# Performance work log

Measured on AMD Instinct MI355X. Metric: run time of the kernel, lower is better.

The kernel has to match this reference:

```python
import jax, jax.numpy as jnp
import numpy as np

N_NODES = 100000
N_EDGES = 3200000
D_IN = 256
D_OUT = 256


def setup_inputs() -> dict:
    key = jax.random.key(0)
    k1, k2, k3, k4, k5 = jax.random.split(key, 5)
    x = jax.random.normal(k1, (N_NODES, D_IN), dtype=jnp.float32)
    # xavier-uniform-like init for weight
    limit = float(np.sqrt(6.0 / (D_IN + D_OUT)))
    weight = jax.random.uniform(k2, (D_IN, D_OUT), dtype=jnp.float32, minval=-limit, maxval=limit)
    edge_val = jax.random.uniform(k3, (N_EDGES,), dtype=jnp.float32)
    edge_row = jax.random.randint(k4, (N_EDGES,), 0, N_NODES, dtype=jnp.int32)
    edge_col = jax.random.randint(k5, (N_EDGES,), 0, N_NODES, dtype=jnp.int32)
    return {"x": x, "weight": weight, "edge_val": edge_val,
            "edge_row": edge_row, "edge_col": edge_col}


def reference(x, weight, edge_val, edge_row, edge_col):
    # dropout p=0.0 -> identity
    support = x @ weight                                  # [N, D_OUT]
    # spmm: out[r] += val * support[c] for each edge (r, c, val)
    msgs = support[edge_col] * edge_val[:, None]          # [E, D_OUT]
    out = jax.ops.segment_sum(msgs, edge_row, num_segments=N_NODES)
    return jax.nn.relu(out)
```

## Files before the change

### kernel.cpp

```cpp
#include <hip/hip_runtime.h>

#define N_NODES 100000
#define N_EDGES 3200000
#define D 256
#define OVF_MAX 8192

#define RPB 128
#define NBUCK 782
#define CAPB 5120
#define SCAP 4608

#define CHUNK 4096
#define NBLK_A ((N_EDGES + CHUNK - 1) / CHUNK)
#define NGRP 196

#define CAST_BLOCKS 6250
#define GEMM_BLOCKS (N_NODES / 16)

typedef __attribute__((ext_vector_type(8))) short bf16x8;
typedef __attribute__((ext_vector_type(4))) float f32x4;

__device__ unsigned short g_wtp[(size_t)16 * 8 * 64 * 8];
__device__ unsigned short g_xb[(size_t)N_NODES * D];
__device__ unsigned       g_y[(size_t)N_NODES * (D / 2)];
__device__ int   g_bucket_cur[NBUCK];
__device__ int2  g_binned[(size_t)NBUCK * CAPB];
__device__ int   g_novf;
__device__ int   g_ovf_row[OVF_MAX];
__device__ int2  g_ovf_edge[OVF_MAX];

__device__ __forceinline__ unsigned short f2bf(float f) {
    unsigned u = __float_as_uint(f);
    unsigned r = u + 0x7fffu + ((u >> 16) & 1u);
    return (unsigned short)(r >> 16);
}

__global__ void setup_kernel(const float* __restrict__ W) {
    const int tid = threadIdx.x;
    if (blockIdx.x < 64) {
        int pb = (blockIdx.x * 256 + tid) * 4;
        #pragma unroll
        for (int j = 0; j < 4; ++j) {
            int p    = pb + j;
            int i8   = p & 7;
            int lane = (p >> 3) & 63;
            int s    = (p >> 9) & 7;
            int nt   = p >> 12;
            int n = nt * 16 + (lane & 15);
            int k = s * 32 + (lane >> 4) * 8 + i8;
            g_wtp[p] = f2bf(W[(size_t)k * D + n]);
        }
    }
    for (int i = blockIdx.x * blockDim.x + tid; i < NBUCK;
         i += gridDim.x * blockDim.x)
        g_bucket_cur[i] = 0;
    if (blockIdx.x == 0 && tid == 0) g_novf = 0;
}

__launch_bounds__(256)
__global__ void bin_cast_kernel(const float* __restrict__ x,
                                const float* __restrict__ edge_val,
                                const int* __restrict__ edge_row,
                                const int* __restrict__ edge_col) {
    __shared__ int2 rec[CHUNK];
    __shared__ unsigned short bid[CHUNK];
    __shared__ int cnt[NGRP * 4];
    __shared__ int pre[NBUCK + 1];
    __shared__ int bas[NBUCK];
    __shared__ int gs[NGRP];
    __shared__ int gofs[NGRP];
    const int tid = threadIdx.x;
    const int b = blockIdx.x;

    if (b < NBLK_A) {
        const int e0 = b * CHUNK;
        for (int q = tid; q < NGRP * 4; q += 256) cnt[q] = 0;
        __syncthreads();
        #pragma unroll
        for (int j = 0; j < CHUNK / 256; ++j) {
            int e = e0 + tid + j * 256;
            if (e < N_EDGES) atomicAdd(&cnt[edge_row[e] >> 7], 1);
        }
        __syncthreads();
        if (tid < NGRP) {
            const int* c = &cnt[tid * 4];
            gs[tid] = c[0] + c[1] + c[2] + c[3];
        }
        __syncthreads();
        if (tid < NGRP) {
            int s = 0;
            for (int j = 0; j < tid; ++j) s += gs[j];
            gofs[tid] = s;
        }
        __syncthreads();
        for (int q = tid; q < NBUCK; q += 256) {
            int p = gofs[q >> 2];
            for (int j = q & ~3; j < q; ++j) p += cnt[j];
            pre[q] = p;
        }
        if (tid == 0) pre[NBUCK] = gofs[NGRP - 1] + gs[NGRP - 1];
        __syncthreads();
        for (int q = tid; q < NBUCK; q += 256)
            bas[q] = cnt[q] ? atomicAdd(&g_bucket_cur[q], cnt[q]) : 0;
        __syncthreads();
        for (int q = tid; q < NGRP * 4; q += 256) cnt[q] = 0;
        __syncthreads();
        #pragma unroll
        for (int j = 0; j < CHUNK / 256; ++j) {
            int e = e0 + tid + j * 256;
            if (e < N_EDGES) {
                int r = edge_row[e];
                int q = r >> 7;
                int o = atomicAdd(&cnt[q], 1);
                int pos = pre[q] + o;
                int2 pk;
                pk.x = edge_col[e] | ((r & 127) << 17);
                pk.y = __float_as_int(edge_val[e]);
                rec[pos] = pk;
                bid[pos] = (unsigned short)q;
            }
        }
        __syncthreads();
        const int total = pre[NBUCK];
        for (int i = tid; i < total; i += 256) {
            int q = bid[i];
            int dest = bas[q] + (i - pre[q]);
            int2 pk = rec[i];
            if (dest < CAPB) {
                g_binned[(size_t)q * CAPB + dest] = pk;
            } else {
                int o = atomicAdd(&g_novf, 1);
                if (o < OVF_MAX) {
                    g_ovf_row[o] = (q << 7) | (pk.x >> 17);
                    int2 ov; ov.x = pk.x & 0x1FFFF; ov.y = pk.y;
                    g_ovf_edge[o] = ov;
                }
            }
        }
    } else {
        const size_t base = (size_t)(b - NBLK_A) * 4096 + (size_t)tid * 16;
        const float4* xp = (const float4*)&x[base];
        float4 f0 = xp[0], f1 = xp[1], f2 = xp[2], f3 = xp[3];
        unsigned short o[16];
        o[ 0]=f2bf(f0.x); o[ 1]=f2bf(f0.y); o[ 2]=f2bf(f0.z); o[ 3]=f2bf(f0.w);
        o[ 4]=f2bf(f1.x); o[ 5]=f2bf(f1.y); o[ 6]=f2bf(f1.z); o[ 7]=f2bf(f1.w);
        o[ 8]=f2bf(f2.x); o[ 9]=f2bf(f2.y); o[10]=f2bf(f2.z); o[11]=f2bf(f2.w);
        o[12]=f2bf(f3.x); o[13]=f2bf(f3.y); o[14]=f2bf(f3.z); o[15]=f2bf(f3.w);
        uint4* dst = (uint4*)&g_xb[base];
        dst[0] = *(const uint4*)&o[0];
        dst[1] = *(const uint4*)&o[8];
    }
}

__launch_bounds__(512)
__global__ void spmm_kernel() {
    __shared__ int2 srec[SCAP];
    __shared__ int rcnt[RPB];
    __shared__ int rofs[RPB];
    __shared__ int rcur[RPB];
    const int k   = blockIdx.x;
    const int tid = threadIdx.x;
    const int nrec_all = min(g_bucket_cur[k], CAPB);
    const int nstage   = min(nrec_all, SCAP);
    const int2* src = &g_binned[(size_t)k * CAPB];

    if (tid < RPB) { rcnt[tid] = 0; rcur[tid] = 0; }
    __syncthreads();
    for (int i = tid; i < nstage; i += 512)
        atomicAdd(&rcnt[src[i].x >> 17], 1);
    __syncthreads();
    if (tid < RPB) {
        int s = 0;
        for (int j = 0; j < tid; ++j) s += rcnt[j];
        rofs[tid] = s;
    }
    __syncthreads();
    for (int i = tid; i < nstage; i += 512) {
        int2 pk = src[i];
        int rl  = pk.x >> 17;
        int pos = rofs[rl] + atomicAdd(&rcur[rl], 1);
        srec[pos] = pk;
    }
    __syncthreads();

    const int grp = tid >> 7;
    const int t   = tid & 127;
    const unsigned* xb = (const unsigned*)g_xb;
    const int novf = min(g_novf, OVF_MAX);

    for (int rr = 0; rr < 32; ++rr) {
        const int rl  = grp * 32 + rr;
        const int row = k * RPB + rl;
        if (row >= N_NODES) break;
        const int cnt = rcnt[rl];
        const int ofs = rofs[rl];
        float a0 = 0.f, a1 = 0.f;
        int i = 0;
        for (; i + 3 < cnt; i += 4) {
            int2 e0 = srec[ofs + i];
            int2 e1 = srec[ofs + i + 1];
            int2 e2 = srec[ofs + i + 2];
            int2 e3 = srec[ofs + i + 3];
            unsigned p0 = xb[(size_t)(e0.x & 0x1FFFF) * (D / 2) + t];
            unsigned p1 = xb[(size_t)(e1.x & 0x1FFFF) * (D / 2) + t];
            unsigned p2 = xb[(size_t)(e2.x & 0x1FFFF) * (D / 2) + t];
            unsigned p3 = xb[(size_t)(e3.x & 0x1FFFF) * (D / 2) + t];
            float v0 = __int_as_float(e0.y);
            float v1 = __int_as_float(e1.y);
            float v2 = __int_as_float(e2.y);
            float v3 = __int_as_float(e3.y);
            a0 += v0 * __uint_as_float(p0 << 16);
            a1 += v0 * __uint_as_float(p0 & 0xffff0000u);
            a0 += v1 * __uint_as_float(p1 << 16);
            a1 += v1 * __uint_as_float(p1 & 0xffff0000u);
            a0 += v2 * __uint_as_float(p2 << 16);
            a1 += v2 * __uint_as_float(p2 & 0xffff0000u);
            a0 += v3 * __uint_as_float(p3 << 16);
            a1 += v3 * __uint_as_float(p3 & 0xffff0000u);
        }
        for (; i < cnt; ++i) {
            int2 e0 = srec[ofs + i];
            unsigned p0 = xb[(size_t)(e0.x & 0x1FFFF) * (D / 2) + t];
            float v0 = __int_as_float(e0.y);
            a0 += v0 * __uint_as_float(p0 << 16);
            a1 += v0 * __uint_as_float(p0 & 0xffff0000u);
        }
        for (int j = nstage; j < nrec_all; ++j) {
            int2 pk = src[j];
            if ((pk.x >> 17) == rl) {
                unsigned p0 = xb[(size_t)(pk.x & 0x1FFFF) * (D / 2) + t];
                float v0 = __int_as_float(pk.y);
                a0 += v0 * __uint_as_float(p0 << 16);
                a1 += v0 * __uint_as_float(p0 & 0xffff0000u);
            }
        }
        if (novf > 0) {
            for (int j = 0; j < novf; ++j) {
                if (g_ovf_row[j] == row) {
                    int2 ee = g_ovf_edge[j];
                    float v0 = __int_as_float(ee.y);
                    unsigned p0 = xb[(size_t)ee.x * (D / 2) + t];
                    a0 += v0 * __uint_as_float(p0 << 16);
                    a1 += v0 * __uint_as_float(p0 & 0xffff0000u);
                }
            }
        }
        g_y[(size_t)row * (D / 2) + t] =
            (unsigned)f2bf(a0) | ((unsigned)f2bf(a1) << 16);
    }
}

__launch_bounds__(256)
__global__ void gemm_kernel(float* __restrict__ out) {
    __shared__ float tile[4][16][68];
    const int g    = blockIdx.x;
    const int wave = threadIdx.x >> 6;
    const int lane = threadIdx.x & 63;
    const int m0   = g * 16;
    const int n0   = wave * 64;
    const int lm   = lane & 15;
    const int q    = lane >> 4;

    const unsigned short* Yb = (const unsigned short*)g_y;
    f32x4 acc0 = {}, acc1 = {}, acc2 = {}, acc3 = {};

    #pragma unroll
    for (int s = 0; s < 8; ++s) {
        bf16x8 av = *(const bf16x8*)&Yb[(size_t)(m0 + lm) * D + s * 32 + q * 8];
        const unsigned short* bp =
            &g_wtp[((size_t)(wave * 4) * 8 + s) * 512 + lane * 8];
        bf16x8 b0 = *(const bf16x8*)&bp[0 * 4096];
        bf16x8 b1 = *(const bf16x8*)&bp[1 * 4096];
        bf16x8 b2 = *(const bf16x8*)&bp[2 * 4096];
        bf16x8 b3 = *(const bf16x8*)&bp[3 * 4096];
        acc0 = __builtin_amdgcn_mfma_f32_16x16x32_bf16(av, b0, acc0, 0, 0, 0);
        acc1 = __builtin_amdgcn_mfma_f32_16x16x32_bf16(av, b1, acc1, 0, 0, 0);
        acc2 = __builtin_amdgcn_mfma_f32_16x16x32_bf16(av, b2, acc2, 0, 0, 0);
        acc3 = __builtin_amdgcn_mfma_f32_16x16x32_bf16(av, b3, acc3, 0, 0, 0);
    }

    #pragma unroll
    for (int r = 0; r < 4; ++r) {
        tile[wave][q * 4 + r][ 0 + lm] = acc0[r];
        tile[wave][q * 4 + r][16 + lm] = acc1[r];
        tile[wave][q * 4 + r][32 + lm] = acc2[r];
        tile[wave][q * 4 + r][48 + lm] = acc3[r];
    }
    const int row  = lane >> 2;
    const int cseg = (lane & 3) * 16;
    float ov[16];
    #pragma unroll
    for (int j = 0; j < 16; ++j)
        ov[j] = fmaxf(tile[wave][row][cseg + j], 0.f);
    float* dst = &out[(size_t)(m0 + row) * D + n0 + cseg];
    #pragma unroll
    for (int j = 0; j < 4; ++j)
        __builtin_nontemporal_store(*(const f32x4*)&ov[j * 4], (f32x4*)&dst[j * 4]);
}

extern "C" void kernel_launch(void* const* d_in, const int* in_sizes, int n_in,
                              void* d_out, int out_size, void* d_ws, size_t ws_size,
                              hipStream_t stream) {
    const float* x        = (const float*)d_in[0];
    const float* weight   = (const float*)d_in[1];
    const float* edge_val = (const float*)d_in[2];
    const int*   edge_row = (const int*)d_in[3];
    const int*   edge_col = (const int*)d_in[4];
    float* out = (float*)d_out;

    setup_kernel<<<64, 256, 0, stream>>>(weight);
    bin_cast_kernel<<<NBLK_A + CAST_BLOCKS, 256, 0, stream>>>(x, edge_val, edge_row, edge_col);
    spmm_kernel<<<NBUCK, 512, 0, stream>>>();
    gemm_kernel<<<GEMM_BLOCKS, 256, 0, stream>>>(out);
}
```

Before: 655.8 us.

## Replace bucketed binning with per-row padded ELL slots via global atomics

Replaces the two-pass, shared-memory bucket sort of edges (782 buckets, with a per-block counting sort inside spmm) with a direct per-row padded layout. Each edge claims a slot with a global atomicAdd on its destination row's cursor, and anything past 64 slots goes to an overflow list. spmm now runs one 128-thread block per row, reading that row's slots directly with nontemporal loads. This removes the shared-memory staging and scan overhead, at the cost of 3.2M contended global atomics, scattered 8-byte writes into a large padded array, and 100k small blocks.

```diff
diff --git a/kernel.cpp b/kernel.cpp
--- a/kernel.cpp
+++ b/kernel.cpp
@@ -3,17 +3,10 @@
 #define N_NODES 100000
 #define N_EDGES 3200000
 #define D 256
+#define CAP 64
 #define OVF_MAX 8192
 
-#define RPB 128
-#define NBUCK 782
-#define CAPB 5120
-#define SCAP 4608
-
-#define CHUNK 4096
-#define NBLK_A ((N_EDGES + CHUNK - 1) / CHUNK)
-#define NGRP 196
-
+#define BUILD_BLOCKS 3125
 #define CAST_BLOCKS 6250
 #define GEMM_BLOCKS (N_NODES / 16)
 
@@ -23,8 +16,8 @@
 __device__ unsigned short g_wtp[(size_t)16 * 8 * 64 * 8];
 __device__ unsigned short g_xb[(size_t)N_NODES * D];
 __device__ unsigned       g_y[(size_t)N_NODES * (D / 2)];
-__device__ int   g_bucket_cur[NBUCK];
-__device__ int2  g_binned[(size_t)NBUCK * CAPB];
+__device__ int   g_cursor[N_NODES];
+__device__ int2  g_pad[(size_t)N_NODES * CAP];
 __device__ int   g_novf;
 __device__ int   g_ovf_row[OVF_MAX];
 __device__ int2  g_ovf_edge[OVF_MAX];
@@ -51,94 +44,39 @@
             g_wtp[p] = f2bf(W[(size_t)k * D + n]);
         }
     }
-    for (int i = blockIdx.x * blockDim.x + tid; i < NBUCK;
+    for (int i = blockIdx.x * blockDim.x + tid; i < N_NODES;
          i += gridDim.x * blockDim.x)
-        g_bucket_cur[i] = 0;
+        g_cursor[i] = 0;
     if (blockIdx.x == 0 && tid == 0) g_novf = 0;
 }
 
 __launch_bounds__(256)
-__global__ void bin_cast_kernel(const float* __restrict__ x,
-                                const float* __restrict__ edge_val,
-                                const int* __restrict__ edge_row,
-                                const int* __restrict__ edge_col) {
-    __shared__ int2 rec[CHUNK];
-    __shared__ unsigned short bid[CHUNK];
-    __shared__ int cnt[NGRP * 4];
-    __shared__ int pre[NBUCK + 1];
-    __shared__ int bas[NBUCK];
-    __shared__ int gs[NGRP];
-    __shared__ int gofs[NGRP];
+__global__ void build_cast_kernel(const float* __restrict__ x,
+                                  const float* __restrict__ edge_val,
+                                  const int* __restrict__ edge_row,
+                                  const int* __restrict__ edge_col) {
     const int tid = threadIdx.x;
     const int b = blockIdx.x;
 
-    if (b < NBLK_A) {
-        const int e0 = b * CHUNK;
-        for (int q = tid; q < NGRP * 4; q += 256) cnt[q] = 0;
-        __syncthreads();
+    if (b < BUILD_BLOCKS) {
+        const int e0 = b * 1024;
         #pragma unroll
-        for (int j = 0; j < CHUNK / 256; ++j) {
-            int e = e0 + tid + j * 256;
-            if (e < N_EDGES) atomicAdd(&cnt[edge_row[e] >> 7], 1);
-        }
-        __syncthreads();
-        if (tid < NGRP) {
-            const int* c = &cnt[tid * 4];
-            gs[tid] = c[0] + c[1] + c[2] + c[3];
-        }
-        __syncthreads();
-        if (tid < NGRP) {
-            int s = 0;
-            for (int j = 0; j < tid; ++j) s += gs[j];
-            gofs[tid] = s;
-        }
-        __syncthreads();
-        for (int q = tid; q < NBUCK; q += 256) {
-            int p = gofs[q >> 2];
-            for (int j = q & ~3; j < q; ++j) p += cnt[j];
-            pre[q] = p;
-        }
-        if (tid == 0) pre[NBUCK] = gofs[NGRP - 1] + gs[NGRP - 1];
-        __syncthreads();
-        for (int q = tid; q < NBUCK; q += 256)
-            bas[q] = cnt[q] ? atomicAdd(&g_bucket_cur[q], cnt[q]) : 0;
-        __syncthreads();
-        for (int q = tid; q < NGRP * 4; q += 256) cnt[q] = 0;
-        __syncthreads();
-        #pragma unroll
-        for (int j = 0; j < CHUNK / 256; ++j) {
-            int e = e0 + tid + j * 256;
-            if (e < N_EDGES) {
-                int r = edge_row[e];
-                int q = r >> 7;
-                int o = atomicAdd(&cnt[q], 1);
-                int pos = pre[q] + o;
-                int2 pk;
-                pk.x = edge_col[e] | ((r & 127) << 17);
-                pk.y = __float_as_int(edge_val[e]);
-                rec[pos] = pk;
-                bid[pos] = (unsigned short)q;
-            }
-        }
-        __syncthreads();
-        const int total = pre[NBUCK];
-        for (int i = tid; i < total; i += 256) {
-            int q = bid[i];
-            int dest = bas[q] + (i - pre[q]);
-            int2 pk = rec[i];
-            if (dest < CAPB) {
-                g_binned[(size_t)q * CAPB + dest] = pk;
+        for (int j = 0; j < 4; ++j) {
+            int e = e0 + j * 256 + tid;
+            int r = edge_row[e];
+            int c = edge_col[e];
+            float v = edge_val[e];
+            int slot = atomicAdd(&g_cursor[r], 1);
+            int2 pk; pk.x = c; pk.y = __float_as_int(v);
+            if (slot < CAP) {
+                g_pad[(size_t)r * CAP + slot] = pk;
             } else {
                 int o = atomicAdd(&g_novf, 1);
-                if (o < OVF_MAX) {
-                    g_ovf_row[o] = (q << 7) | (pk.x >> 17);
-                    int2 ov; ov.x = pk.x & 0x1FFFF; ov.y = pk.y;
-                    g_ovf_edge[o] = ov;
-                }
+                if (o < OVF_MAX) { g_ovf_row[o] = r; g_ovf_edge[o] = pk; }
             }
         }
     } else {
-        const size_t base = (size_t)(b - NBLK_A) * 4096 + (size_t)tid * 16;
+        const size_t base = (size_t)(b - BUILD_BLOCKS) * 4096 + (size_t)tid * 16;
         const float4* xp = (const float4*)&x[base];
         float4 f0 = xp[0], f1 = xp[1], f2 = xp[2], f3 = xp[3];
         unsigned short o[16];
@@ -152,102 +90,60 @@
     }
 }
 
-__launch_bounds__(512)
+__launch_bounds__(128)
 __global__ void spmm_kernel() {
-    __shared__ int2 srec[SCAP];
-    __shared__ int rcnt[RPB];
-    __shared__ int rofs[RPB];
-    __shared__ int rcur[RPB];
-    const int k   = blockIdx.x;
-    const int tid = threadIdx.x;
-    const int nrec_all = min(g_bucket_cur[k], CAPB);
-    const int nstage   = min(nrec_all, SCAP);
-    const int2* src = &g_binned[(size_t)k * CAPB];
-
-    if (tid < RPB) { rcnt[tid] = 0; rcur[tid] = 0; }
-    __syncthreads();
-    for (int i = tid; i < nstage; i += 512)
-        atomicAdd(&rcnt[src[i].x >> 17], 1);
-    __syncthreads();
-    if (tid < RPB) {
-        int s = 0;
-        for (int j = 0; j < tid; ++j) s += rcnt[j];
-        rofs[tid] = s;
-    }
-    __syncthreads();
-    for (int i = tid; i < nstage; i += 512) {
-        int2 pk = src[i];
-        int rl  = pk.x >> 17;
-        int pos = rofs[rl] + atomicAdd(&rcur[rl], 1);
-        srec[pos] = pk;
-    }
-    __syncthreads();
-
-    const int grp = tid >> 7;
-    const int t   = tid & 127;
+    const int r = blockIdx.x;
+    const int t = threadIdx.x;
+    const int deg = g_cursor[r];
+    const int dpad = min(deg, CAP);
+    const long long* rowp = (const long long*)&g_pad[(size_t)r * CAP];
     const unsigned* xb = (const unsigned*)g_xb;
+
+    float a0 = 0.f, a1 = 0.f;
+    int i = 0;
+    for (; i + 3 < dpad; i += 4) {
+        long long q0 = __builtin_nontemporal_load(&rowp[i]);
+        long long q1 = __builtin_nontemporal_load(&rowp[i + 1]);
+        long long q2 = __builtin_nontemporal_load(&rowp[i + 2]);
+        long long q3 = __builtin_nontemporal_load(&rowp[i + 3]);
+        unsigned p0 = xb[(size_t)(int)q0 * (D / 2) + t];
+        unsigned p1 = xb[(size_t)(int)q1 * (D / 2) + t];
+        unsigned p2 = xb[(size_t)(int)q2 * (D / 2) + t];
+        unsigned p3 = xb[(size_t)(int)q3 * (D / 2) + t];
+        float v0 = __int_as_float((int)(q0 >> 32));
+        float v1 = __int_as_float((int)(q1 >> 32));
+        float v2 = __int_as_float((int)(q2 >> 32));
+        float v3 = __int_as_float((int)(q3 >> 32));
+        a0 += v0 * __uint_as_float(p0 << 16);
+        a1 += v0 * __uint_as_float(p0 & 0xffff0000u);
+        a0 += v1 * __uint_as_float(p1 << 16);
+        a1 += v1 * __uint_as_float(p1 & 0xffff0000u);
+        a0 += v2 * __uint_as_float(p2 << 16);
+        a1 += v2 * __uint_as_float(p2 & 0xffff0000u);
+        a0 += v3 * __uint_as_float(p3 << 16);
+        a1 += v3 * __uint_as_float(p3 & 0xffff0000u);
+    }
+    for (; i < dpad; ++i) {
+        long long q0 = __builtin_nontemporal_load(&rowp[i]);
+        float v0 = __int_as_float((int)(q0 >> 32));
+        unsigned p0 = xb[(size_t)(int)q0 * (D / 2) + t];
+        a0 += v0 * __uint_as_float(p0 << 16);
+        a1 += v0 * __uint_as_float(p0 & 0xffff0000u);
+    }
     const int novf = min(g_novf, OVF_MAX);
-
-    for (int rr = 0; rr < 32; ++rr) {
-        const int rl  = grp * 32 + rr;
-        const int row = k * RPB + rl;
-        if (row >= N_NODES) break;
-        const int cnt = rcnt[rl];
-        const int ofs = rofs[rl];
-        float a0 = 0.f, a1 = 0.f;
-        int i = 0;
-        for (; i + 3 < cnt; i += 4) {
-            int2 e0 = srec[ofs + i];
-            int2 e1 = srec[ofs + i + 1];
-            int2 e2 = srec[ofs + i + 2];
-            int2 e3 = srec[ofs + i + 3];
-            unsigned p0 = xb[(size_t)(e0.x & 0x1FFFF) * (D / 2) + t];
-            unsigned p1 = xb[(size_t)(e1.x & 0x1FFFF) * (D / 2) + t];
-            unsigned p2 = xb[(size_t)(e2.x & 0x1FFFF) * (D / 2) + t];
-            unsigned p3 = xb[(size_t)(e3.x & 0x1FFFF) * (D / 2) + t];
-            float v0 = __int_as_float(e0.y);
-            float v1 = __int_as_float(e1.y);
-            float v2 = __int_as_float(e2.y);
-            float v3 = __int_as_float(e3.y);
-            a0 += v0 * __uint_as_float(p0 << 16);
-            a1 += v0 * __uint_as_float(p0 & 0xffff0000u);
-            a0 += v1 * __uint_as_float(p1 << 16);
-            a1 += v1 * __uint_as_float(p1 & 0xffff0000u);
-            a0 += v2 * __uint_as_float(p2 << 16);
-            a1 += v2 * __uint_as_float(p2 & 0xffff0000u);
-            a0 += v3 * __uint_as_float(p3 << 16);
-            a1 += v3 * __uint_as_float(p3 & 0xffff0000u);
-        }
-        for (; i < cnt; ++i) {
-            int2 e0 = srec[ofs + i];
-            unsigned p0 = xb[(size_t)(e0.x & 0x1FFFF) * (D / 2) + t];
-            float v0 = __int_as_float(e0.y);
-            a0 += v0 * __uint_as_float(p0 << 16);
-            a1 += v0 * __uint_as_float(p0 & 0xffff0000u);
-        }
-        for (int j = nstage; j < nrec_all; ++j) {
-            int2 pk = src[j];
-            if ((pk.x >> 17) == rl) {
-                unsigned p0 = xb[(size_t)(pk.x & 0x1FFFF) * (D / 2) + t];
-                float v0 = __int_as_float(pk.y);
+    if (novf > 0) {
+        for (int j = 0; j < novf; ++j) {
+            if (g_ovf_row[j] == r) {
+                int2 e0 = g_ovf_edge[j];
+                float v0 = __int_as_float(e0.y);
+                unsigned p0 = xb[(size_t)e0.x * (D / 2) + t];
                 a0 += v0 * __uint_as_float(p0 << 16);
                 a1 += v0 * __uint_as_float(p0 & 0xffff0000u);
             }
         }
-        if (novf > 0) {
-            for (int j = 0; j < novf; ++j) {
-                if (g_ovf_row[j] == row) {
-                    int2 ee = g_ovf_edge[j];
-                    float v0 = __int_as_float(ee.y);
-                    unsigned p0 = xb[(size_t)ee.x * (D / 2) + t];
-                    a0 += v0 * __uint_as_float(p0 << 16);
-                    a1 += v0 * __uint_as_float(p0 & 0xffff0000u);
-                }
-            }
-        }
-        g_y[(size_t)row * (D / 2) + t] =
-            (unsigned)f2bf(a0) | ((unsigned)f2bf(a1) << 16);
-    }
+    }
+    g_y[(size_t)r * (D / 2) + t] =
+        (unsigned)f2bf(a0) | ((unsigned)f2bf(a1) << 16);
 }
 
 __launch_bounds__(256)
@@ -309,7 +205,8 @@
     float* out = (float*)d_out;
 
     setup_kernel<<<64, 256, 0, stream>>>(weight);
-    bin_cast_kernel<<<NBLK_A + CAST_BLOCKS, 256, 0, stream>>>(x, edge_val, edge_row, edge_col);
-    spmm_kernel<<<NBUCK, 512, 0, stream>>>();
+    build_cast_kernel<<<BUILD_BLOCKS + CAST_BLOCKS, 256, 0, stream>>>(
+        x, edge_val, edge_row, edge_col);
+    spmm_kernel<<<N_NODES, 128, 0, stream>>>();
     gemm_kernel<<<GEMM_BLOCKS, 256, 0, stream>>>(out);
 }
```

Result: no change. 667.9 us (+1.8%).
